# Performance work log

Hardware: AMD Instinct MI355X
Metric: run time of the kernel (lower is better)

Reference implementation:

```python
import jax, jax.numpy as jnp
import numpy as np

N = 8192      # nodes in g
M = 16384     # line-graph nodes (feat_b rows)
E = 131072    # edges (avg degree 16)
IN = 128
OUT = 128
RADIUS = 3


def setup_inputs() -> dict:
    key = jax.random.key(0)
    ks = jax.random.split(key, 20)
    s = 1.0 / np.sqrt(IN)
    sf = 1.0 / np.sqrt(2 * IN)
    inp = {
        "feat_a": jax.random.normal(ks[0], (N, IN), jnp.float32),
        "feat_b": jax.random.normal(ks[1], (M, IN), jnp.float32),
        "deg": jax.random.uniform(ks[2], (N, 1), jnp.float32) * 16.0,
        "pm_pd": jax.random.normal(ks[3], (N, M, 2), jnp.float32) * 0.01,
        "src": jax.random.randint(ks[4], (E,), 0, N, jnp.int32),
        "dst": jax.random.randint(ks[5], (E,), 0, N, jnp.int32),
        "W_prev": jax.random.uniform(ks[6], (IN, OUT), jnp.float32, -s, s),
        "b_prev": jax.random.uniform(ks[7], (OUT,), jnp.float32, -s, s),
        "W_deg": jax.random.uniform(ks[8], (IN, OUT), jnp.float32, -s, s),
        "b_deg": jax.random.uniform(ks[9], (OUT,), jnp.float32, -s, s),
        "W_r": jax.random.uniform(ks[10], (RADIUS, IN, OUT), jnp.float32, -s, s),
        "b_r": jax.random.uniform(ks[11], (RADIUS, OUT), jnp.float32, -s, s),
        "W_fuse": jax.random.uniform(ks[12], (2 * IN, OUT), jnp.float32, -sf, sf),
        "b_fuse": jax.random.uniform(ks[13], (OUT,), jnp.float32, -sf, sf),
        "gamma": jnp.ones((OUT,), jnp.float32),
        "beta": jnp.zeros((OUT,), jnp.float32),
    }
    return inp


def reference(feat_a, feat_b, deg, pm_pd, src, dst,
              W_prev, b_prev, W_deg, b_deg, W_r, b_r,
              W_fuse, b_fuse, gamma, beta):
    # one round of copy_src + sum message passing (SpMM with edge list)
    def agg(z):
        return jax.ops.segment_sum(z[src], dst, num_segments=N)

    # aggregate_radius: z_list[k] = A^{2^k} feat_a for k = 0..radius-1
    z = agg(feat_a)
    z_list = [z]
    for i in range(RADIUS - 1):
        for _ in range(2 ** i):
            z = agg(z)
        z_list.append(z)

    prev_proj = feat_a @ W_prev + b_prev
    deg_proj = (deg * feat_a) @ W_deg + b_deg
    radius_proj = sum(z_list[k] @ W_r[k] + b_r[k] for k in range(RADIUS))

    # dense pm_pd fusion: [N, M] @ [M, IN] twice, concat on feature dim
    fuse_in = jnp.concatenate(
        [pm_pd[:, :, 0] @ feat_b, pm_pd[:, :, 1] @ feat_b], axis=1)
    fuse = fuse_in @ W_fuse + b_fuse

    result = prev_proj + deg_proj + radius_proj + fuse
    n = OUT // 2
    result = jnp.concatenate(
        [result[:, :n], jax.nn.relu(result[:, n:])], axis=1)

    # BatchNorm1d, training mode (batch statistics, biased variance)
    mean = jnp.mean(result, axis=0)
    var = jnp.var(result, axis=0)
    out = (result - mean) * jax.lax.rsqrt(var + 1e-5) * gamma + beta
    return out
```

## Files before the change

### kernel.cpp

```cpp
#include <hip/hip_runtime.h>
#include <hip/hip_bf16.h>

#define NN 8192
#define MM 16384
#define EE 131072
#define K2 32768

typedef unsigned short u16;
typedef unsigned int u32;
typedef __attribute__((ext_vector_type(8))) short bf16x8;
typedef __attribute__((ext_vector_type(4))) float f32x4;
typedef __attribute__((ext_vector_type(4))) float f4;

__device__ __forceinline__ u16 f2bf(float f){
  union { float f; unsigned u; } x; x.f = f;
  return (u16)((x.u + 0x7FFFu + ((x.u >> 16) & 1u)) >> 16);
}

__device__ __forceinline__ bf16x8 cvt8(f4 a, f4 b){
  bf16x8 r;
  r[0]=(short)f2bf(a.x); r[1]=(short)f2bf(a.y);
  r[2]=(short)f2bf(a.z); r[3]=(short)f2bf(a.w);
  r[4]=(short)f2bf(b.x); r[5]=(short)f2bf(b.y);
  r[6]=(short)f2bf(b.z); r[7]=(short)f2bf(b.w);
  return r;
}

__device__ __forceinline__ bf16x8 cvt8t(f4 a, f4 b){
  union { u32 u[4]; bf16x8 v; } r;
  r.u[0] = __builtin_amdgcn_perm(__float_as_uint(a.y), __float_as_uint(a.x), 0x07060302u);
  r.u[1] = __builtin_amdgcn_perm(__float_as_uint(a.w), __float_as_uint(a.z), 0x07060302u);
  r.u[2] = __builtin_amdgcn_perm(__float_as_uint(b.y), __float_as_uint(b.x), 0x07060302u);
  r.u[3] = __builtin_amdgcn_perm(__float_as_uint(b.w), __float_as_uint(b.z), 0x07060302u);
  return r.v;
}

__global__ void wft_k(const float* __restrict__ W_fuse, u16* __restrict__ WfT){
  int co = blockIdx.x, j = threadIdx.x;
  int c = co >> 7, o = co & 127;
  WfT[co*128 + j] = f2bf(W_fuse[(c*128 + j)*128 + o]);
}

__global__ __launch_bounds__(128) void prep_bpt(const float* __restrict__ feat_b,
                                                const u16* __restrict__ WfT,
                                                u32* __restrict__ BpT32){
  int t = threadIdx.x, w = t >> 6, l = t & 63;
  int lr = l & 15, lk = l >> 4;
  int mrow = blockIdx.x*32 + w*16;
  f32x4 acc[16] = {};
  const float* ap = feat_b + (size_t)(mrow + lr)*128 + lk*8;
  #pragma unroll
  for (int ks = 0; ks < 4; ++ks){
    f4 a0 = *(const f4*)(ap + ks*32);
    f4 a1 = *(const f4*)(ap + ks*32 + 4);
    bf16x8 a = cvt8(a0, a1);
    #pragma unroll
    for (int cf = 0; cf < 16; ++cf){
      bf16x8 b = *(const bf16x8*)(WfT + (cf*16 + lr)*128 + ks*32 + lk*8);
      acc[cf] = __builtin_amdgcn_mfma_f32_16x16x32_bf16(a, b, acc[cf], 0, 0, 0);
    }
  }
  #pragma unroll
  for (int cf = 0; cf < 8; ++cf){
    int o = cf*16 + lr;
    uint4 v;
    v.x = (u32)f2bf(acc[cf][0]) | ((u32)f2bf(acc[cf+8][0]) << 16);
    v.y = (u32)f2bf(acc[cf][1]) | ((u32)f2bf(acc[cf+8][1]) << 16);
    v.z = (u32)f2bf(acc[cf][2]) | ((u32)f2bf(acc[cf+8][2]) << 16);
    v.w = (u32)f2bf(acc[cf][3]) | ((u32)f2bf(acc[cf+8][3]) << 16);
    *(uint4*)(BpT32 + (size_t)o*16384 + mrow + lk*4) = v;
  }
}

__global__ void hist_k(const int* __restrict__ dst, int* __restrict__ hist){
  int e = blockIdx.x*256 + threadIdx.x;
  atomicAdd(hist + dst[e], 1);
}

__global__ void scan_k(const int* __restrict__ hist, int* __restrict__ off,
                       int* __restrict__ cursor){
  __shared__ int part[256];
  int t = threadIdx.x;
  int loc[32]; int s = 0;
  #pragma unroll
  for (int i = 0; i < 32; ++i){ loc[i] = hist[t*32 + i]; s += loc[i]; }
  part[t] = s;
  __syncthreads();
  for (int d = 1; d < 256; d <<= 1){
    int v = (t >= d) ? part[t-d] : 0;
    __syncthreads();
    part[t] += v;
    __syncthreads();
  }
  int run = (t > 0) ? part[t-1] : 0;
  #pragma unroll
  for (int i = 0; i < 32; ++i){ off[t*32+i] = run; cursor[t*32+i] = run; run += loc[i]; }
  if (t == 255) off[NN] = run;
}

__global__ void fill_k(const int* __restrict__ src, const int* __restrict__ dst,
                       int* __restrict__ cursor, int* __restrict__ eidx){
  int e = blockIdx.x*256 + threadIdx.x;
  int pos = atomicAdd(cursor + dst[e], 1);
  eidx[pos] = src[e];
}

__global__ __launch_bounds__(256) void agg_k(const float* __restrict__ zin,
                                             float* __restrict__ zout,
                                             const int* __restrict__ off,
                                             const int* __restrict__ eidx){
  int t = threadIdx.x;
  int node = blockIdx.x*8 + (t >> 5);
  int c = (t & 31)*4;
  int s = off[node], e = off[node+1];
  float a0=0.f, a1=0.f, a2=0.f, a3=0.f;
  for (int j = s; j < e; ++j){
    f4 v = *(const f4*)(zin + (size_t)eidx[j]*128 + c);
    a0 += v.x; a1 += v.y; a2 += v.z; a3 += v.w;
  }
  f4 r; r.x=a0; r.y=a1; r.z=a2; r.w=a3;
  *(f4*)(zout + (size_t)node*128 + c) = r;
}

__global__ __launch_bounds__(256) void proj_all(
    const float* __restrict__ feat_a, const float* __restrict__ deg,
    const float* __restrict__ z0, const float* __restrict__ z1, const float* __restrict__ z2,
    const float* __restrict__ W_prev, const float* __restrict__ W_deg, const float* __restrict__ W_r,
    const float* __restrict__ b_prev, const float* __restrict__ b_deg,
    const float* __restrict__ b_r, const float* __restrict__ b_fuse,
    float* __restrict__ out)
{
  __shared__ float Xs[32][64];
  __shared__ float Ws[64][128];
  int t = threadIdx.x;
  int rbase = blockIdx.x*32;
  int o0 = (t & 15)*8, r0 = (t >> 4)*2;
  float acc[2][8] = {};
  for (int p = 0; p < 10; ++p){
    int seg = p >> 1, half = p & 1;
    {
      int row = t >> 3, e8 = t & 7;
      const float* bp = (seg <= 1) ? feat_a : (seg == 2) ? z0 : (seg == 3) ? z1 : z2;
      const float* sp = bp + (size_t)(rbase+row)*128 + half*64 + e8*8;
      f4 v0 = *(const f4*)sp;
      f4 v1 = *(const f4*)(sp+4);
      if (seg == 1){
        float d = deg[rbase+row];
        v0 *= d; v1 *= d;
      }
      *(f4*)&Xs[row][e8*8]   = v0;
      *(f4*)&Xs[row][e8*8+4] = v1;
    }
    #pragma unroll
    for (int it = 0; it < 8; ++it){
      int lin = it*1024 + t*4;
      int wr = lin >> 7, wc = lin & 127;
      int ksrc = p*64 + wr;
      int sg = ksrc >> 7, kin = ksrc & 127;
      const float* wp = (sg == 0) ? W_prev : (sg == 1) ? W_deg : (W_r + (size_t)(sg-2)*16384);
      *(f4*)&Ws[wr][wc] = *(const f4*)(wp + kin*128 + wc);
    }
    __syncthreads();
    #pragma unroll 8
    for (int kk = 0; kk < 64; ++kk){
      float x0 = Xs[r0][kk], x1 = Xs[r0+1][kk];
      f4 wa = *(const f4*)&Ws[kk][o0];
      f4 wb = *(const f4*)&Ws[kk][o0+4];
      acc[0][0]=fmaf(x0,wa.x,acc[0][0]); acc[0][1]=fmaf(x0,wa.y,acc[0][1]);
      acc[0][2]=fmaf(x0,wa.z,acc[0][2]); acc[0][3]=fmaf(x0,wa.w,acc[0][3]);
      acc[0][4]=fmaf(x0,wb.x,acc[0][4]); acc[0][5]=fmaf(x0,wb.y,acc[0][5]);
      acc[0][6]=fmaf(x0,wb.z,acc[0][6]); acc[0][7]=fmaf(x0,wb.w,acc[0][7]);
      acc[1][0]=fmaf(x1,wa.x,acc[1][0]); acc[1][1]=fmaf(x1,wa.y,acc[1][1]);
      acc[1][2]=fmaf(x1,wa.z,acc[1][2]); acc[1][3]=fmaf(x1,wa.w,acc[1][3]);
      acc[1][4]=fmaf(x1,wb.x,acc[1][4]); acc[1][5]=fmaf(x1,wb.y,acc[1][5]);
      acc[1][6]=fmaf(x1,wb.z,acc[1][6]); acc[1][7]=fmaf(x1,wb.w,acc[1][7]);
    }
    __syncthreads();
  }
  #pragma unroll
  for (int i = 0; i < 2; ++i){
    int r = rbase + r0 + i;
    #pragma unroll
    for (int j = 0; j < 8; ++j){
      int o = o0 + j;
      float bias = b_prev[o] + b_deg[o] + b_fuse[o] + b_r[o] + b_r[128+o] + b_r[256+o];
      out[(size_t)r*128 + o] = acc[i][j] + bias;
    }
  }
}

__global__ __launch_bounds__(256, 2) void fuse_gemm(const float* __restrict__ A,
                                                    const u16* __restrict__ BpT,
                                                    float* __restrict__ out){
  __shared__ u16 Bs[128*64];
  int b = blockIdx.x;
  int rowtile = b & 63, kc = b >> 6;
  int t = threadIdx.x, w = t >> 6, l = t & 63;
  int lr = l & 15, lk = l >> 4;
  size_t kbase = (size_t)kc*4096;
  int row0 = rowtile*128 + w*32 + lr;
  const float* a0p = A + (size_t)row0*K2 + kbase + lk*8;
  const float* a1p = a0p + (size_t)16*K2;
  f32x4 acc[2][8] = {};
  for (int tile = 0; tile < 64; ++tile){
    size_t kt = kbase + tile*64;
    #pragma unroll
    for (int pp = 0; pp < 4; ++pp){
      int q = pp*256 + t;
      int o = q >> 3, oct = q & 7;
      uint4 v = *(const uint4*)(BpT + (size_t)o*K2 + kt + oct*8);
      *(uint4*)((char*)Bs + o*128 + ((oct ^ (o & 7)) << 4)) = v;
    }
    __syncthreads();
    #pragma unroll
    for (int s = 0; s < 2; ++s){
      const float* pa0 = a0p + tile*64 + s*32;
      const float* pa1 = a1p + tile*64 + s*32;
      f4 x0 = __builtin_nontemporal_load((const f4*)pa0);
      f4 x1 = __builtin_nontemporal_load((const f4*)pa0 + 1);
      f4 y0 = __builtin_nontemporal_load((const f4*)pa1);
      f4 y1 = __builtin_nontemporal_load((const f4*)pa1 + 1);
      bf16x8 a0 = cvt8t(x0, x1);
      bf16x8 a1 = cvt8t(y0, y1);
      int khalf = s*4 + lk;
      #pragma unroll
      for (int cf = 0; cf < 8; ++cf){
        int o = cf*16 + lr;
        bf16x8 bfr = *(const bf16x8*)((char*)Bs + o*128 + ((khalf ^ (o & 7)) << 4));
        acc[0][cf] = __builtin_amdgcn_mfma_f32_16x16x32_bf16(a0, bfr, acc[0][cf], 0, 0, 0);
        acc[1][cf] = __builtin_amdgcn_mfma_f32_16x16x32_bf16(a1, bfr, acc[1][cf], 0, 0, 0);
      }
    }
    __syncthreads();
  }
  int orow = rowtile*128 + w*32 + lk*4;
  #pragma unroll
  for (int rf = 0; rf < 2; ++rf){
    #pragma unroll
    for (int cf = 0; cf < 8; ++cf){
      #pragma unroll
      for (int j = 0; j < 4; ++j){
        unsafeAtomicAdd(out + (size_t)(orow + rf*16 + j)*128 + cf*16 + lr, acc[rf][cf][j]);
      }
    }
  }
}

__global__ __launch_bounds__(256) void colstats(const float* __restrict__ acc,
                                                float* __restrict__ gsum,
                                                float* __restrict__ gsumsq){
  __shared__ float s1[8][128], s2[8][128];
  int t = threadIdx.x;
  int c4 = (t & 31)*4, rsub = t >> 5;
  int rbase = blockIdx.x*32;
  f4 sum = {0,0,0,0}, sq = {0,0,0,0};
  #pragma unroll
  for (int i = 0; i < 4; ++i){
    f4 v = *(const f4*)(acc + (size_t)(rbase + rsub + i*8)*128 + c4);
    if (c4 >= 64){
      v.x=fmaxf(v.x,0.f); v.y=fmaxf(v.y,0.f); v.z=fmaxf(v.z,0.f); v.w=fmaxf(v.w,0.f);
    }
    sum += v; sq += v*v;
  }
  *(f4*)&s1[rsub][c4] = sum;
  *(f4*)&s2[rsub][c4] = sq;
  __syncthreads();
  if (t < 128){
    float a = 0.f, b2 = 0.f;
    #pragma unroll
    for (int r = 0; r < 8; ++r){ a += s1[r][t]; b2 += s2[r][t]; }
    unsafeAtomicAdd(gsum + t, a);
    unsafeAtomicAdd(gsumsq + t, b2);
  }
}

__global__ void bn_final(const float* __restrict__ gsum, const float* __restrict__ gsumsq,
                         const float* __restrict__ gamma, const float* __restrict__ beta,
                         float* __restrict__ scale, float* __restrict__ shift){
  int c = threadIdx.x;
  float mean = gsum[c] * (1.f/8192.f);
  float var  = gsumsq[c] * (1.f/8192.f) - mean*mean;
  float rstd = rsqrtf(var + 1e-5f);
  float sc = rstd * gamma[c];
  scale[c] = sc;
  shift[c] = beta[c] - mean*sc;
}

__global__ __launch_bounds__(256) void bn_apply(float* __restrict__ out,
                                                const float* __restrict__ scale,
                                                const float* __restrict__ shift){
  int i = blockIdx.x*256 + threadIdx.x;
  int j = i & 31;
  f4* o4 = (f4*)out;
  f4 v = o4[i];
  if (j >= 16){
    v.x=fmaxf(v.x,0.f); v.y=fmaxf(v.y,0.f); v.z=fmaxf(v.z,0.f); v.w=fmaxf(v.w,0.f);
  }
  f4 sc = *(const f4*)(scale + j*4);
  f4 sh = *(const f4*)(shift + j*4);
  v.x = fmaf(v.x,sc.x,sh.x); v.y = fmaf(v.y,sc.y,sh.y);
  v.z = fmaf(v.z,sc.z,sh.z); v.w = fmaf(v.w,sc.w,sh.w);
  o4[i] = v;
}

extern "C" void kernel_launch(void* const* d_in, const int* in_sizes, int n_in,
                              void* d_out, int out_size, void* d_ws, size_t ws_size,
                              hipStream_t stream) {
  const float* feat_a = (const float*)d_in[0];
  const float* feat_b = (const float*)d_in[1];
  const float* deg    = (const float*)d_in[2];
  const float* pm_pd  = (const float*)d_in[3];
  const int*   src    = (const int*)d_in[4];
  const int*   dst    = (const int*)d_in[5];
  const float* W_prev = (const float*)d_in[6];
  const float* b_prev = (const float*)d_in[7];
  const float* W_deg  = (const float*)d_in[8];
  const float* b_deg  = (const float*)d_in[9];
  const float* W_r    = (const float*)d_in[10];
  const float* b_r    = (const float*)d_in[11];
  const float* W_fuse = (const float*)d_in[12];
  const float* b_fuse = (const float*)d_in[13];
  const float* gamma  = (const float*)d_in[14];
  const float* beta   = (const float*)d_in[15];
  float* out = (float*)d_out;

  char* w = (char*)d_ws;
  u16*   BpT    = (u16*)  (w + 0);
  float* z0     = (float*)(w + 8388608);
  float* z1     = (float*)(w + 12582912);
  float* ztmp   = (float*)(w + 16777216);
  float* z2     = (float*)(w + 20971520);
  u16*   WfT    = (u16*)  (w + 25165824);
  int*   hist   = (int*)  (w + 25231360);
  int*   off    = (int*)  (w + 25264128);
  int*   cursor = (int*)  (w + 25296912);
  int*   eidx   = (int*)  (w + 25329680);
  float* gsum   = (float*)(w + 25853968);
  float* gsumsq = gsum + 128;
  float* scale  = (float*)(w + 25854992);
  float* shift  = (float*)(w + 25855504);
  if (ws_size < (size_t)25856016) return;

  hipMemsetAsync(hist, 0, NN*sizeof(int), stream);
  hipMemsetAsync(gsum, 0, 256*sizeof(float), stream);

  wft_k<<<256, 128, 0, stream>>>(W_fuse, WfT);
  prep_bpt<<<MM/32, 128, 0, stream>>>(feat_b, WfT, (u32*)BpT);

  hist_k<<<EE/256, 256, 0, stream>>>(dst, hist);
  scan_k<<<1, 256, 0, stream>>>(hist, off, cursor);
  fill_k<<<EE/256, 256, 0, stream>>>(src, dst, cursor, eidx);

  agg_k<<<NN/8, 256, 0, stream>>>(feat_a, z0, off, eidx);
  agg_k<<<NN/8, 256, 0, stream>>>(z0, z1, off, eidx);
  agg_k<<<NN/8, 256, 0, stream>>>(z1, ztmp, off, eidx);
  agg_k<<<NN/8, 256, 0, stream>>>(ztmp, z2, off, eidx);

  proj_all<<<NN/32, 256, 0, stream>>>(feat_a, deg, z0, z1, z2,
                                      W_prev, W_deg, W_r, b_prev, b_deg, b_r, b_fuse, out);

  fuse_gemm<<<512, 256, 0, stream>>>(pm_pd, BpT, out);

  colstats<<<NN/32, 256, 0, stream>>>(out, gsum, gsumsq);
  bn_final<<<1, 128, 0, stream>>>(gsum, gsumsq, gamma, beta, scale, shift);
  bn_apply<<<NN*128/4/256, 256, 0, stream>>>(out, scale, shift);
}
```

Before: 443.8 us.

## Pre-pack B in MFMA fragment order and drop LDS staging in fuse GEMM

prep_bpt now writes the projected feat_b operand directly in per-lane MFMA fragment order, so fuse_gemm loads its B fragments straight from global memory with no LDS tile or __syncthreads. The K dimension is split into twice as many chunks (1024 blocks) so more blocks share the streaming of pm_pd, and the two-per-CU occupancy hint is dropped. This removes LDS traffic and barrier stalls but relies on L2/cache for B reuse across waves, and it doubles the atomic adds into the output.

```diff
diff --git a/kernel.cpp b/kernel.cpp
--- a/kernel.cpp
+++ b/kernel.cpp
@@ -43,7 +43,7 @@
 
 __global__ __launch_bounds__(128) void prep_bpt(const float* __restrict__ feat_b,
                                                 const u16* __restrict__ WfT,
-                                                u32* __restrict__ BpT32){
+                                                char* __restrict__ Bpack){
   int t = threadIdx.x, w = t >> 6, l = t & 63;
   int lr = l & 15, lk = l >> 4;
   int mrow = blockIdx.x*32 + w*16;
@@ -60,6 +60,7 @@
       acc[cf] = __builtin_amdgcn_mfma_f32_16x16x32_bf16(a, b, acc[cf], 0, 0, 0);
     }
   }
+  char* dstb = Bpack + (size_t)(mrow >> 4)*8192 + lk*16;
   #pragma unroll
   for (int cf = 0; cf < 8; ++cf){
     int o = cf*16 + lr;
@@ -68,7 +69,7 @@
     v.y = (u32)f2bf(acc[cf][1]) | ((u32)f2bf(acc[cf+8][1]) << 16);
     v.z = (u32)f2bf(acc[cf][2]) | ((u32)f2bf(acc[cf+8][2]) << 16);
     v.w = (u32)f2bf(acc[cf][3]) | ((u32)f2bf(acc[cf+8][3]) << 16);
-    *(uint4*)(BpT32 + (size_t)o*16384 + mrow + lk*4) = v;
+    *(uint4*)(dstb + o*64) = v;
   }
 }
 
@@ -189,49 +190,34 @@
   }
 }
 
-__global__ __launch_bounds__(256, 2) void fuse_gemm(const float* __restrict__ A,
-                                                    const u16* __restrict__ BpT,
-                                                    float* __restrict__ out){
-  __shared__ u16 Bs[128*64];
+__global__ __launch_bounds__(256) void fuse_gemm(const float* __restrict__ A,
+                                                 const char* __restrict__ Bpack,
+                                                 float* __restrict__ out){
   int b = blockIdx.x;
   int rowtile = b & 63, kc = b >> 6;
   int t = threadIdx.x, w = t >> 6, l = t & 63;
   int lr = l & 15, lk = l >> 4;
-  size_t kbase = (size_t)kc*4096;
   int row0 = rowtile*128 + w*32 + lr;
-  const float* a0p = A + (size_t)row0*K2 + kbase + lk*8;
+  const float* a0p = A + (size_t)row0*K2 + kc*2048 + lk*8;
   const float* a1p = a0p + (size_t)16*K2;
+  const char* bp = Bpack + (size_t)(kc*64)*8192 + lr*64 + lk*16;
   f32x4 acc[2][8] = {};
   for (int tile = 0; tile < 64; ++tile){
-    size_t kt = kbase + tile*64;
-    #pragma unroll
-    for (int pp = 0; pp < 4; ++pp){
-      int q = pp*256 + t;
-      int o = q >> 3, oct = q & 7;
-      uint4 v = *(const uint4*)(BpT + (size_t)o*K2 + kt + oct*8);
-      *(uint4*)((char*)Bs + o*128 + ((oct ^ (o & 7)) << 4)) = v;
-    }
-    __syncthreads();
-    #pragma unroll
-    for (int s = 0; s < 2; ++s){
-      const float* pa0 = a0p + tile*64 + s*32;
-      const float* pa1 = a1p + tile*64 + s*32;
-      f4 x0 = __builtin_nontemporal_load((const f4*)pa0);
-      f4 x1 = __builtin_nontemporal_load((const f4*)pa0 + 1);
-      f4 y0 = __builtin_nontemporal_load((const f4*)pa1);
-      f4 y1 = __builtin_nontemporal_load((const f4*)pa1 + 1);
-      bf16x8 a0 = cvt8t(x0, x1);
-      bf16x8 a1 = cvt8t(y0, y1);
-      int khalf = s*4 + lk;
-      #pragma unroll
-      for (int cf = 0; cf < 8; ++cf){
-        int o = cf*16 + lr;
-        bf16x8 bfr = *(const bf16x8*)((char*)Bs + o*128 + ((khalf ^ (o & 7)) << 4));
-        acc[0][cf] = __builtin_amdgcn_mfma_f32_16x16x32_bf16(a0, bfr, acc[0][cf], 0, 0, 0);
-        acc[1][cf] = __builtin_amdgcn_mfma_f32_16x16x32_bf16(a1, bfr, acc[1][cf], 0, 0, 0);
-      }
-    }
-    __syncthreads();
+    const float* pa0 = a0p + tile*32;
+    const float* pa1 = a1p + tile*32;
+    f4 x0 = __builtin_nontemporal_load((const f4*)pa0);
+    f4 x1 = __builtin_nontemporal_load((const f4*)pa0 + 1);
+    f4 y0 = __builtin_nontemporal_load((const f4*)pa1);
+    f4 y1 = __builtin_nontemporal_load((const f4*)pa1 + 1);
+    bf16x8 a0 = cvt8t(x0, x1);
+    bf16x8 a1 = cvt8t(y0, y1);
+    const char* bt = bp + (size_t)tile*8192;
+    #pragma unroll
+    for (int cf = 0; cf < 8; ++cf){
+      bf16x8 bfr = *(const bf16x8*)(bt + cf*1024);
+      acc[0][cf] = __builtin_amdgcn_mfma_f32_16x16x32_bf16(a0, bfr, acc[0][cf], 0, 0, 0);
+      acc[1][cf] = __builtin_amdgcn_mfma_f32_16x16x32_bf16(a1, bfr, acc[1][cf], 0, 0, 0);
+    }
   }
   int orow = rowtile*128 + w*32 + lk*4;
   #pragma unroll
@@ -325,7 +311,7 @@
   float* out = (float*)d_out;
 
   char* w = (char*)d_ws;
-  u16*   BpT    = (u16*)  (w + 0);
+  char*  Bpack  = (char*) (w + 0);
   float* z0     = (float*)(w + 8388608);
   float* z1     = (float*)(w + 12582912);
   float* ztmp   = (float*)(w + 16777216);
@@ -345,7 +331,7 @@
   hipMemsetAsync(gsum, 0, 256*sizeof(float), stream);
 
   wft_k<<<256, 128, 0, stream>>>(W_fuse, WfT);
-  prep_bpt<<<MM/32, 128, 0, stream>>>(feat_b, WfT, (u32*)BpT);
+  prep_bpt<<<MM/32, 128, 0, stream>>>(feat_b, WfT, Bpack);
 
   hist_k<<<EE/256, 256, 0, stream>>>(dst, hist);
   scan_k<<<1, 256, 0, stream>>>(hist, off, cursor);
@@ -359,7 +345,7 @@
   proj_all<<<NN/32, 256, 0, stream>>>(feat_a, deg, z0, z1, z2,
                                       W_prev, W_deg, W_r, b_prev, b_deg, b_r, b_fuse, out);
 
-  fuse_gemm<<<512, 256, 0, stream>>>(pm_pd, BpT, out);
+  fuse_gemm<<<1024, 256, 0, stream>>>(pm_pd, Bpack, out);
 
   colstats<<<NN/32, 256, 0, stream>>>(out, gsum, gsumsq);
   bn_final<<<1, 128, 0, stream>>>(gsum, gsumsq, gamma, beta, scale, shift);
```

Result: slower. 675.6 us (+52.3%).
